# Kernel optimization log

Measured on AMD Instinct MI355X. Metric: run time of the kernel, lower is better.

The kernel has to match this reference:

```python
import jax, jax.numpy as jnp
import numpy as np

N_BINS = 15
N = 20_000_000


def setup_inputs() -> dict:
    key = jax.random.key(0)
    k1, k2, k3 = jax.random.split(key, 3)
    preds = jax.random.randint(k1, (N,), 0, 1000, dtype=jnp.int64)
    targets = jax.random.randint(k2, (N,), 0, 1000, dtype=jnp.int64)
    confs = jax.random.uniform(k3, (N,), dtype=jnp.float32)
    return {"preds": preds, "targets": targets, "confs": confs}


def reference(preds, targets, confs):
    n = confs.shape[0]
    acc = (preds == targets).astype(confs.dtype)
    # bin i covers (i/n_bins, (i+1)/n_bins]; conf <= 0 falls in no bin
    idx = jnp.ceil(confs * N_BINS).astype(jnp.int32) - 1
    valid = idx >= 0
    idx = jnp.where(valid, idx, 0)
    w = valid.astype(confs.dtype)
    count = jax.ops.segment_sum(w, idx, num_segments=N_BINS)
    conf_sum = jax.ops.segment_sum(confs * w, idx, num_segments=N_BINS)
    acc_sum = jax.ops.segment_sum(acc * w, idx, num_segments=N_BINS)
    prop = count / n
    safe = jnp.maximum(count, 1.0)
    gap = jnp.abs(conf_sum / safe - acc_sum / safe)
    ece = jnp.sum(jnp.where(count > 0, gap * prop, 0.0))
    return ece.reshape(1)
```

## Files before the change

kernel.cpp:

```cpp
#include <hip/hip_runtime.h>

#define ECE_BINS 15
#define NSUB 32

__global__ __launch_bounds__(256) void ece_accum_kernel(
    const int* __restrict__ preds,
    const int* __restrict__ targets,
    const float* __restrict__ confs,
    int n,
    unsigned long long* __restrict__ g_cntacc,
    unsigned long long* __restrict__ g_conf)
{
    __shared__ unsigned long long s_cntacc[ECE_BINS][NSUB];
    __shared__ unsigned long long s_conf[ECE_BINS][NSUB];

    for (int i = threadIdx.x; i < ECE_BINS * NSUB; i += 256) {
        (&s_cntacc[0][0])[i] = 0ull;
        (&s_conf[0][0])[i]   = 0ull;
    }
    __syncthreads();

    const int  sub      = threadIdx.x & (NSUB - 1);
    const long tid      = (long)blockIdx.x * 256 + threadIdx.x;
    const long nthreads = (long)gridDim.x * 256;

    const int nvec = n >> 2;
    const int4*   p4 = (const int4*)preds;
    const int4*   t4 = (const int4*)targets;
    const float4* c4 = (const float4*)confs;

    for (long i = tid; i < nvec; i += nthreads) {
        int4   p = p4[i];
        int4   t = t4[i];
        float4 c = c4[i];
        const int   pv[4] = {p.x, p.y, p.z, p.w};
        const int   tv[4] = {t.x, t.y, t.z, t.w};
        const float cv[4] = {c.x, c.y, c.z, c.w};
        #pragma unroll
        for (int j = 0; j < 4; ++j) {
            int idx = (int)ceilf(cv[j] * 15.0f) - 1;
            if (idx >= 0) {
                idx = idx > (ECE_BINS - 1) ? (ECE_BINS - 1) : idx;
                unsigned long long inc = 1ull + ((pv[j] == tv[j]) ? (1ull << 32) : 0ull);
                atomicAdd(&s_cntacc[idx][sub], inc);
                unsigned long long cf = (unsigned long long)((double)cv[j] * 4294967296.0);
                atomicAdd(&s_conf[idx][sub], cf);
            }
        }
    }
    for (long i = (long)(nvec << 2) + tid; i < n; i += nthreads) {
        int idx = (int)ceilf(confs[i] * 15.0f) - 1;
        if (idx >= 0) {
            idx = idx > (ECE_BINS - 1) ? (ECE_BINS - 1) : idx;
            unsigned long long inc = 1ull + ((preds[i] == targets[i]) ? (1ull << 32) : 0ull);
            atomicAdd(&s_cntacc[idx][sub], inc);
            unsigned long long cf = (unsigned long long)((double)confs[i] * 4294967296.0);
            atomicAdd(&s_conf[idx][sub], cf);
        }
    }

    __syncthreads();
    if (threadIdx.x < ECE_BINS) {
        unsigned long long ca = 0ull, cf = 0ull;
        #pragma unroll
        for (int s = 0; s < NSUB; ++s) {
            ca += s_cntacc[threadIdx.x][s];
            cf += s_conf[threadIdx.x][s];
        }
        atomicAdd(&g_cntacc[threadIdx.x], ca);
        atomicAdd(&g_conf[threadIdx.x], cf);
    }
}

__global__ void ece_final_kernel(const unsigned long long* __restrict__ g_cntacc,
                                 const unsigned long long* __restrict__ g_conf,
                                 float* __restrict__ out, int n)
{
    if (threadIdx.x == 0 && blockIdx.x == 0) {
        double ece = 0.0;
        for (int b = 0; b < ECE_BINS; ++b) {
            unsigned long long ca = g_cntacc[b];
            double cnt  = (double)(unsigned int)(ca & 0xffffffffull);
            double acc  = (double)(unsigned int)(ca >> 32);
            double csum = (double)g_conf[b] * (1.0 / 4294967296.0);
            if (cnt > 0.0) {
                double gap = fabs(csum / cnt - acc / cnt);
                ece += gap * (cnt / (double)n);
            }
        }
        out[0] = (float)ece;
    }
}

extern "C" void kernel_launch(void* const* d_in, const int* in_sizes, int n_in,
                              void* d_out, int out_size, void* d_ws, size_t ws_size,
                              hipStream_t stream) {
    const int*   preds   = (const int*)d_in[0];
    const int*   targets = (const int*)d_in[1];
    const float* confs   = (const float*)d_in[2];
    float*       out     = (float*)d_out;
    const int    n       = in_sizes[2];

    unsigned long long* g_cntacc = (unsigned long long*)d_ws;
    unsigned long long* g_conf   = g_cntacc + ECE_BINS;

    hipMemsetAsync(d_ws, 0, 2 * ECE_BINS * sizeof(unsigned long long), stream);

    ece_accum_kernel<<<2048, 256, 0, stream>>>(preds, targets, confs, n, g_cntacc, g_conf);
    ece_final_kernel<<<1, 64, 0, stream>>>(g_cntacc, g_conf, out, n);
}
```

Baseline: 263.7 us.

## Replace shared-memory atomics with per-thread register bins and fuse finalize

Each thread now keeps 15 bin counters and 15 double confidence sums in registers, updated by predicated adds over all bins, so the per-element 64-bit shared-memory atomics go away. Block totals are combined through a two-stage shared-memory tree and added to global memory with atomics. The last block to finish, detected with an atomic ticket, computes the ECE, which removes the separate finalize kernel launch. The grid shrinks to 768 blocks. The trade is 15x more ALU work per element plus high register pressure from the double accumulators, and the 16-bit packed per-thread counters could overflow on larger inputs.

```diff
diff --git a/kernel.cpp b/kernel.cpp
--- a/kernel.cpp
+++ b/kernel.cpp
@@ -1,94 +1,108 @@
 #include <hip/hip_runtime.h>
 
 #define ECE_BINS 15
-#define NSUB 32
+#define NTHREADS 256
+#define NBLOCKS  768
 
-__global__ __launch_bounds__(256) void ece_accum_kernel(
+__global__ __launch_bounds__(256) void ece_fused_kernel(
     const int* __restrict__ preds,
     const int* __restrict__ targets,
     const float* __restrict__ confs,
     int n,
-    unsigned long long* __restrict__ g_cntacc,
-    unsigned long long* __restrict__ g_conf)
+    unsigned long long* __restrict__ ws,
+    float* __restrict__ out)
 {
-    __shared__ unsigned long long s_cntacc[ECE_BINS][NSUB];
-    __shared__ unsigned long long s_conf[ECE_BINS][NSUB];
+    unsigned cnt[ECE_BINS];
+    double   cf[ECE_BINS];
+    #pragma unroll
+    for (int b = 0; b < ECE_BINS; ++b) { cnt[b] = 0u; cf[b] = 0.0; }
 
-    for (int i = threadIdx.x; i < ECE_BINS * NSUB; i += 256) {
-        (&s_cntacc[0][0])[i] = 0ull;
-        (&s_conf[0][0])[i]   = 0ull;
-    }
-    __syncthreads();
-
-    const int  sub      = threadIdx.x & (NSUB - 1);
-    const long tid      = (long)blockIdx.x * 256 + threadIdx.x;
-    const long nthreads = (long)gridDim.x * 256;
-
+    const long tid = (long)blockIdx.x * NTHREADS + threadIdx.x;
+    const long S   = (long)gridDim.x * NTHREADS;
     const int nvec = n >> 2;
     const int4*   p4 = (const int4*)preds;
     const int4*   t4 = (const int4*)targets;
     const float4* c4 = (const float4*)confs;
 
-    for (long i = tid; i < nvec; i += nthreads) {
-        int4   p = p4[i];
-        int4   t = t4[i];
-        float4 c = c4[i];
+    for (long i = tid; i < nvec; i += S) {
+        int4 p = p4[i]; int4 t = t4[i]; float4 c = c4[i];
         const int   pv[4] = {p.x, p.y, p.z, p.w};
         const int   tv[4] = {t.x, t.y, t.z, t.w};
         const float cv[4] = {c.x, c.y, c.z, c.w};
         #pragma unroll
         for (int j = 0; j < 4; ++j) {
             int idx = (int)ceilf(cv[j] * 15.0f) - 1;
-            if (idx >= 0) {
-                idx = idx > (ECE_BINS - 1) ? (ECE_BINS - 1) : idx;
-                unsigned long long inc = 1ull + ((pv[j] == tv[j]) ? (1ull << 32) : 0ull);
-                atomicAdd(&s_cntacc[idx][sub], inc);
-                unsigned long long cf = (unsigned long long)((double)cv[j] * 4294967296.0);
-                atomicAdd(&s_conf[idx][sub], cf);
+            unsigned inc = (pv[j] == tv[j]) ? 0x10001u : 1u;
+            double qd = trunc((double)cv[j] * 4294967296.0);
+            #pragma unroll
+            for (int b = 0; b < ECE_BINS; ++b) {
+                bool m = (idx == b);
+                cnt[b] += m ? inc : 0u;
+                cf[b]  += m ? qd : 0.0;
             }
         }
     }
-    for (long i = (long)(nvec << 2) + tid; i < n; i += nthreads) {
-        int idx = (int)ceilf(confs[i] * 15.0f) - 1;
-        if (idx >= 0) {
-            idx = idx > (ECE_BINS - 1) ? (ECE_BINS - 1) : idx;
-            unsigned long long inc = 1ull + ((preds[i] == targets[i]) ? (1ull << 32) : 0ull);
-            atomicAdd(&s_cntacc[idx][sub], inc);
-            unsigned long long cf = (unsigned long long)((double)confs[i] * 4294967296.0);
-            atomicAdd(&s_conf[idx][sub], cf);
+    for (long k = ((long)nvec << 2) + tid; k < n; k += S) {
+        int idx = (int)ceilf(confs[k] * 15.0f) - 1;
+        unsigned inc = (preds[k] == targets[k]) ? 0x10001u : 1u;
+        double qd = trunc((double)confs[k] * 4294967296.0);
+        #pragma unroll
+        for (int b = 0; b < ECE_BINS; ++b) {
+            bool m = (idx == b);
+            cnt[b] += m ? inc : 0u;
+            cf[b]  += m ? qd : 0.0;
         }
     }
 
+    __shared__ unsigned s_cnt[NTHREADS][ECE_BINS];
+    __shared__ double   s_cf [NTHREADS][ECE_BINS];
+    #pragma unroll
+    for (int b = 0; b < ECE_BINS; ++b) {
+        s_cnt[threadIdx.x][b] = cnt[b];
+        s_cf [threadIdx.x][b] = cf[b];
+    }
     __syncthreads();
+
+    unsigned c1 = 0; double d1 = 0.0; int b1 = 0, k1 = 0;
+    if (threadIdx.x < 240) {
+        b1 = threadIdx.x % 15; k1 = threadIdx.x / 15;
+        #pragma unroll
+        for (int m = 0; m < 16; ++m) {
+            c1 += s_cnt[k1 * 16 + m][b1];
+            d1 += s_cf [k1 * 16 + m][b1];
+        }
+    }
+    __syncthreads();
+    if (threadIdx.x < 240) { s_cnt[k1][b1] = c1; s_cf[k1][b1] = d1; }
+    __syncthreads();
+
     if (threadIdx.x < ECE_BINS) {
-        unsigned long long ca = 0ull, cf = 0ull;
+        const int b = threadIdx.x;
+        unsigned cs = 0; double ds = 0.0;
         #pragma unroll
-        for (int s = 0; s < NSUB; ++s) {
-            ca += s_cntacc[threadIdx.x][s];
-            cf += s_conf[threadIdx.x][s];
+        for (int m = 0; m < 16; ++m) { cs += s_cnt[m][b]; ds += s_cf[m][b]; }
+        unsigned long long count = cs & 0xFFFFu;
+        unsigned long long corr  = cs >> 16;
+        atomicAdd(&ws[b],      count | (corr << 32));
+        atomicAdd(&ws[15 + b], (unsigned long long)ds);
+        __threadfence();
+    }
+    __syncthreads();
+
+    if (threadIdx.x == 0) {
+        unsigned long long t = atomicAdd(&ws[30], 1ull);
+        if (t == (unsigned long long)gridDim.x - 1ull) {
+            double ece = 0.0;
+            for (int b = 0; b < ECE_BINS; ++b) {
+                unsigned long long ca = atomicAdd(&ws[b], 0ull);
+                unsigned long long cq = atomicAdd(&ws[15 + b], 0ull);
+                double c = (double)(unsigned)(ca & 0xffffffffull);
+                double a = (double)(unsigned)(ca >> 32);
+                double s = (double)cq * (1.0 / 4294967296.0);
+                if (c > 0.0) ece += fabs(s / c - a / c) * (c / (double)n);
+            }
+            out[0] = (float)ece;
         }
-        atomicAdd(&g_cntacc[threadIdx.x], ca);
-        atomicAdd(&g_conf[threadIdx.x], cf);
-    }
-}
-
-__global__ void ece_final_kernel(const unsigned long long* __restrict__ g_cntacc,
-                                 const unsigned long long* __restrict__ g_conf,
-                                 float* __restrict__ out, int n)
-{
-    if (threadIdx.x == 0 && blockIdx.x == 0) {
-        double ece = 0.0;
-        for (int b = 0; b < ECE_BINS; ++b) {
-            unsigned long long ca = g_cntacc[b];
-            double cnt  = (double)(unsigned int)(ca & 0xffffffffull);
-            double acc  = (double)(unsigned int)(ca >> 32);
-            double csum = (double)g_conf[b] * (1.0 / 4294967296.0);
-            if (cnt > 0.0) {
-                double gap = fabs(csum / cnt - acc / cnt);
-                ece += gap * (cnt / (double)n);
-            }
-        }
-        out[0] = (float)ece;
     }
 }
 
@@ -101,11 +115,9 @@
     float*       out     = (float*)d_out;
     const int    n       = in_sizes[2];
 
-    unsigned long long* g_cntacc = (unsigned long long*)d_ws;
-    unsigned long long* g_conf   = g_cntacc + ECE_BINS;
+    unsigned long long* ws = (unsigned long long*)d_ws;
 
-    hipMemsetAsync(d_ws, 0, 2 * ECE_BINS * sizeof(unsigned long long), stream);
+    hipMemsetAsync(ws, 0, 31 * sizeof(unsigned long long), stream);
 
-    ece_accum_kernel<<<2048, 256, 0, stream>>>(preds, targets, confs, n, g_cntacc, g_conf);
-    ece_final_kernel<<<1, 64, 0, stream>>>(g_cntacc, g_conf, out, n);
+    ece_fused_kernel<<<NBLOCKS, NTHREADS, 0, stream>>>(preds, targets, confs, n, ws, out);
 }
```

Result: no change. 269.0 us (+2.0%).
